# Kernel optimization log

Measured on AMD Instinct MI355X. Metric: run time of the kernel, lower is better.

The kernel has to match this reference:

```python
import jax, jax.numpy as jnp
import numpy as np

EPS = 1e-5
EXTEND_SCOPE = 1.0

def conv2d(x, w, b, pad):
    out = jax.lax.conv_general_dilated(x, w, (1, 1), [(pad, pad), (pad, pad)],
                                       dimension_numbers=('NCHW', 'OIHW', 'NCHW'))
    return out + b[None, :, None, None]

def group_norm(x, groups, gamma, beta):
    B, C, H, W = x.shape
    xg = x.reshape(B, groups, -1)
    mu = xg.mean(-1, keepdims=True)
    var = xg.var(-1, keepdims=True)
    xn = ((xg - mu) * jax.lax.rsqrt(var + EPS)).reshape(B, C, H, W)
    return xn * gamma[None, :, None, None] + beta[None, :, None, None]

def bilinear_sample(feat, y, x):
    # feat [B,C,H,W]; y,x pixel coords [B,Ho,Wo]; zeros padding, align_corners=True
    B, C, H, W = feat.shape
    flat = feat.reshape(B, C, H * W)
    y0 = jnp.floor(y); x0 = jnp.floor(x)
    wy = (y - y0)[:, None]; wx = (x - x0)[:, None]  # [B,1,Ho,Wo]
    y0i = y0.astype(jnp.int32); x0i = x0.astype(jnp.int32)
    Ho, Wo = y.shape[1], y.shape[2]
    def gather(yi, xi):
        valid = ((yi >= 0) & (yi < H) & (xi >= 0) & (xi < W)).astype(feat.dtype)[:, None]
        idx = (jnp.clip(yi, 0, H - 1) * W + jnp.clip(xi, 0, W - 1)).reshape(B, -1)
        g = jax.vmap(lambda f, i: f[:, i])(flat, idx).reshape(B, C, Ho, Wo)
        return g * valid
    g00 = gather(y0i, x0i)
    g01 = gather(y0i, x0i + 1)
    g10 = gather(y0i + 1, x0i)
    g11 = gather(y0i + 1, x0i + 1)
    return g00 * (1 - wy) * (1 - wx) + g01 * (1 - wy) * wx + g10 * wy * (1 - wx) + g11 * wy * wx

def setup_inputs() -> dict:
    key = jax.random.key(0)
    ks = jax.random.split(key, 4)
    B, C, H, W, K, O = 4, 64, 128, 128, 9, 64
    return {
        'x': jax.random.normal(ks[0], (B, C, H, W), jnp.float32),
        'w_off': jax.random.normal(ks[1], (K, C, 3, 3), jnp.float32) * 0.05,
        'b_off': jnp.zeros((K,), jnp.float32),
        'w_theta': jax.random.normal(ks[2], (K, C, 5, 5), jnp.float32) * 0.05,
        'b_theta': jnp.zeros((K,), jnp.float32),
        'gn_off_g': jnp.ones((K,), jnp.float32),
        'gn_off_b': jnp.zeros((K,), jnp.float32),
        'gn_th_g': jnp.ones((K,), jnp.float32),
        'gn_th_b': jnp.zeros((K,), jnp.float32),
        'w_strip': jax.random.normal(ks[3], (O, C, K, 1), jnp.float32) * 0.05,
        'b_strip': jnp.zeros((O,), jnp.float32),
        'gn_out_g': jnp.ones((O,), jnp.float32),
        'gn_out_b': jnp.zeros((O,), jnp.float32),
    }

def reference(x, w_off, b_off, w_theta, b_theta, gn_off_g, gn_off_b,
              gn_th_g, gn_th_b, w_strip, b_strip, gn_out_g, gn_out_b):
    B, C, H, W = x.shape
    K = w_off.shape[0]
    center = K // 2
    off = jnp.tanh(group_norm(conv2d(x, w_off, b_off, 1), 3, gn_off_g, gn_off_b))       # [B,K,H,W]
    th = jnp.arctan(group_norm(conv2d(x, w_theta, b_theta, 2), 3, gn_th_g, gn_th_b))    # [B,K,H,W]
    k = jnp.arange(K)
    s = (k - center).astype(x.dtype)[None, :, None, None]   # signed kernel offset
    m = center + jnp.abs(k - center)                        # mirror index (uses theta/offset at center+|i|)
    th_m = th[:, m]; off_m = off[:, m]                      # [B,K,H,W]
    is_center = (k == center)[None, :, None, None]
    y_off = jnp.where(is_center, 0.0, s * jnp.tan(th_m) + off_m * jnp.cos(th_m))
    x_off = jnp.where(is_center, 0.0, s - jnp.sin(th_m) * off_m)
    y_new = jnp.arange(H, dtype=x.dtype)[None, None, :, None] + s + EXTEND_SCOPE * y_off
    x_new = jnp.arange(W, dtype=x.dtype)[None, None, None, :] + s + EXTEND_SCOPE * x_off
    # rearrange 'b k h w -> b (h k) w'
    y_map = y_new.transpose(0, 2, 1, 3).reshape(B, H * K, W)
    x_map = x_new.transpose(0, 2, 1, 3).reshape(B, H * K, W)
    # clamp to valid range; scale to [-1,1] + align_corners=True grid_sample is identity in pixel space
    y_map = jnp.clip(y_map, 0.0, float(H - 1))
    x_map = jnp.clip(x_map, 0.0, float(W - 1))
    deformed = bilinear_sample(x, y_map, x_map)             # [B,C,K*H,W]
    d = deformed.reshape(B, C, H, K, W)
    out = jnp.einsum('bchkw,ock->bohw', d, w_strip[..., 0]) + b_strip[None, :, None, None]
    O = w_strip.shape[0]
    out = jax.nn.relu(group_norm(out, O // 4, gn_out_g, gn_out_b))
    return out
```

## Files before the change

kernel.cpp:

```cpp
#include <hip/hip_runtime.h>
#include <math.h>


typedef short v8s __attribute__((ext_vector_type(8)));
typedef float v4f __attribute__((ext_vector_type(4)));

__device__ __forceinline__ float fast_tanh(float a) {
    float aa = fabsf(a);
    float e = __expf(2.f * aa);
    float t = 1.f - 2.f / (e + 1.f);
    return copysignf(t, a);
}

__global__ __launch_bounds__(256) void k_pack(
    const float* __restrict__ w_strip, short* __restrict__ w_pack)
{
    int idx = blockIdx.x * 256 + threadIdx.x;
    int j    = idx & 7;
    int lane = (idx >> 3) & 63;
    int kk   = (idx >> 9) & 1;
    int wv   = (idx >> 10) & 3;
    int k    = idx >> 12;
    int c = (kk << 5) + ((lane >> 4) << 3) + j;
    int o = (wv << 4) + (lane & 15);
    union { short s; __bf16 h; } u;
    u.h = (__bf16)w_strip[(o * 64 + c) * 9 + k];
    w_pack[idx] = u.s;
}

__global__ __launch_bounds__(256) void k_tr(
    const float* __restrict__ x, float* __restrict__ xt)
{
    __shared__ float l[64][65];
    const int t    = threadIdx.x;
    const int lane = t & 63;
    const int wv   = t >> 6;
    const int b    = blockIdx.x >> 8;
    const int pix0 = (blockIdx.x & 255) << 6;

#pragma unroll
    for (int it = 0; it < 16; ++it) {
        int c = (wv << 4) + it;
        l[lane][c] = x[(((size_t)(b << 6) + c) << 14) + pix0 + lane];
    }
    __syncthreads();
#pragma unroll
    for (int it = 0; it < 4; ++it) {
        int idx = (it << 8) + t;
        int p  = idx >> 4;
        int c4 = (idx & 15) << 2;
        float4 v = { l[p][c4], l[p][c4 + 1], l[p][c4 + 2], l[p][c4 + 3] };
        *(float4*)(xt + (((size_t)(b << 14) + pix0 + p) << 6) + c4) = v;
    }
}

__global__ __launch_bounds__(256, 8) void k_conv(
    const float* __restrict__ x,
    const float* __restrict__ w_off, const float* __restrict__ b_off,
    const float* __restrict__ w_th,  const float* __restrict__ b_th,
    float* __restrict__ off_raw, float* __restrict__ th_raw)
{
    __shared__ float tile[12][36];
    const int t  = threadIdx.x;
    const int tx = t & 31, ty = t >> 5;
    const int z  = blockIdx.z;
    const int b  = z >> 3, sp = z & 7;
    const int c0 = sp << 3;
    const int h0 = blockIdx.y << 3, w0 = blockIdx.x << 5;

    float accO[9], accT[9];
#pragma unroll
    for (int k = 0; k < 9; ++k) { accO[k] = 0.f; accT[k] = 0.f; }

    for (int ci = 0; ci < 8; ++ci) {
        const int c = c0 + ci;
        __syncthreads();
        const float* xp = x + (((size_t)(b << 6) + c) << 14);
        for (int e = t; e < 432; e += 256) {
            int r = e / 36, cc = e - r * 36;
            int hh = h0 + r - 2, ww = w0 + cc - 2;
            tile[r][cc] = (hh >= 0 && hh < 128 && ww >= 0 && ww < 128)
                            ? xp[(hh << 7) + ww] : 0.f;
        }
        __syncthreads();

        float win[5][5];
#pragma unroll
        for (int i = 0; i < 5; ++i)
#pragma unroll
            for (int j = 0; j < 5; ++j)
                win[i][j] = tile[ty + i][tx + j];

#pragma unroll
        for (int k = 0; k < 9; ++k) {
            const float* wo = w_off + (size_t)((k << 6) + c) * 9;
            float a = accO[k];
#pragma unroll
            for (int i = 0; i < 3; ++i)
#pragma unroll
                for (int j = 0; j < 3; ++j)
                    a = fmaf(win[i + 1][j + 1], wo[i * 3 + j], a);
            accO[k] = a;

            const float* wt = w_th + (size_t)((k << 6) + c) * 25;
            float bb = accT[k];
#pragma unroll
            for (int i = 0; i < 5; ++i)
#pragma unroll
                for (int j = 0; j < 5; ++j)
                    bb = fmaf(win[i][j], wt[i * 5 + j], bb);
            accT[k] = bb;
        }
    }

    const int pix = ((h0 + ty) << 7) + (w0 + tx);
#pragma unroll
    for (int k = 0; k < 9; ++k) {
        float vo = accO[k] + (sp == 0 ? b_off[k] : 0.f);
        float vt = accT[k] + (sp == 0 ? b_th[k]  : 0.f);
        atomicAdd(&off_raw[((b * 9 + k) << 14) + pix], vo);
        atomicAdd(&th_raw [((b * 9 + k) << 14) + pix], vt);
    }
}

__global__ __launch_bounds__(256) void k_stats(
    const float* __restrict__ off_raw, const float* __restrict__ th_raw,
    float* __restrict__ stats)
{
    const int id  = blockIdx.x;
    const int arr = id >= 36;
    const int rem = id - arr * 36;
    const float4* src = (const float4*)((arr ? th_raw : off_raw) + (rem << 14));

    float s1 = 0.f, s2 = 0.f;
    for (int i = threadIdx.x; i < 4096; i += 256) {
        float4 v = src[i];
        s1 += v.x + v.y + v.z + v.w;
        s2 += v.x * v.x + v.y * v.y + v.z * v.z + v.w * v.w;
    }
#pragma unroll
    for (int d = 32; d; d >>= 1) { s1 += __shfl_down(s1, d, 64); s2 += __shfl_down(s2, d, 64); }

    __shared__ float ls1[4], ls2[4];
    const int wv = threadIdx.x >> 6;
    if ((threadIdx.x & 63) == 0) { ls1[wv] = s1; ls2[wv] = s2; }
    __syncthreads();
    if (threadIdx.x == 0) {
        stats[arr * 72 + rem]      = ls1[0] + ls1[1] + ls1[2] + ls1[3];
        stats[arr * 72 + 36 + rem] = ls2[0] + ls2[1] + ls2[2] + ls2[3];
    }
}

__global__ __launch_bounds__(256, 8) void k_sample_strip2(
    const float* __restrict__ xt,
    const float* __restrict__ off_raw, const float* __restrict__ th_raw,
    const float* __restrict__ stats,
    const float* __restrict__ g_off, const float* __restrict__ be_off,
    const float* __restrict__ g_th,  const float* __restrict__ be_th,
    const short* __restrict__ w_pack, const float* __restrict__ b_strip,
    float* __restrict__ out, float* __restrict__ out_stats)
{
    __shared__ __align__(16) short smem[2][2048];
    const int t    = threadIdx.x;
    const int lane = t & 63;
    const int wv   = __builtin_amdgcn_readfirstlane(t >> 6);
    const int bid  = blockIdx.x;
    const int blk  = ((bid & 7) << 8) + (bid >> 3);
    const int b    = blk >> 9;
    const int pix0 = (blk & 511) << 5;
    const int l32  = lane & 31;
    const int q    = lane >> 5;
    const int p_img = pix0 + l32;
    const int h    = p_img >> 7, w = p_img & 127;
    const int i15  = lane & 15, lg = lane >> 4;
    const int c0   = (wv << 4) + (q << 3);
    const int cb   = (wv << 1) + q;

    float muO[3], isO[3], muT[3], isT[3];
    const float inv_cnt = 1.f / (3.f * 16384.f);
#pragma unroll
    for (int g = 0; g < 3; ++g) {
        float s = 0.f, qq = 0.f;
#pragma unroll
        for (int j = 0; j < 3; ++j) { s += stats[b * 9 + 3 * g + j]; qq += stats[36 + b * 9 + 3 * g + j]; }
        float mu = s * inv_cnt;
        muO[g] = mu; isO[g] = rsqrtf(fmaxf(qq * inv_cnt - mu * mu, 0.f) + 1e-5f);
        s = 0.f; qq = 0.f;
#pragma unroll
        for (int j = 0; j < 3; ++j) { s += stats[72 + b * 9 + 3 * g + j]; qq += stats[108 + b * 9 + 3 * g + j]; }
        mu = s * inv_cnt;
        muT[g] = mu; isT[g] = rsqrtf(fmaxf(qq * inv_cnt - mu * mu, 0.f) + 1e-5f);
    }

    const float* xtb = xt + ((size_t)(b << 14) << 6);

    v4f acc[2];
    acc[0] = (v4f)0.f; acc[1] = (v4f)0.f;
    int cur = 0;

    for (int k = 0; k < 9; ++k) {
        float vv[8];
        if (k == 4) {
            const float* src = xtb + ((size_t)p_img << 6) + c0;
            float4 A = *(const float4*)src;
            float4 Bv = *(const float4*)(src + 4);
            vv[0] = A.x;  vv[1] = A.y;  vv[2] = A.z;  vv[3] = A.w;
            vv[4] = Bv.x; vv[5] = Bv.y; vv[6] = Bv.z; vv[7] = Bv.w;
        } else {
            const int s = k - 4;
            const int m = 4 + (s < 0 ? -s : s);
            const int g = m / 3;
            float z = (th_raw[((b * 9 + m) << 14) + p_img] - muT[g]) * isT[g] * g_th[m] + be_th[m];
            float f = fast_tanh((off_raw[((b * 9 + m) << 14) + p_img] - muO[g]) * isO[g] * g_off[m] + be_off[m]);
            float r = rsqrtf(1.f + z * z);
            float fs = (float)s;
            float yy = (float)h + fs + fs * z + f * r;
            float xx = (float)w + fs + fs - z * r * f;
            yy = fminf(fmaxf(yy, 0.f), 127.f);
            xx = fminf(fmaxf(xx, 0.f), 127.f);
            int y0 = min((int)yy, 126);
            int x0 = min((int)xx, 126);
            float wy = yy - (float)y0;
            float wx = xx - (float)x0;
            const float* base = xtb + ((size_t)((y0 << 7) + x0) << 6) + c0;
#pragma unroll
            for (int hf = 0; hf < 2; ++hf) {
                const float* bp = base + (hf << 2);
                float4 c00 = *(const float4*)bp;
                float4 c01 = *(const float4*)(bp + 64);
                float4 c10 = *(const float4*)(bp + 8192);
                float4 c11 = *(const float4*)(bp + 8256);
                float tx0 = fmaf(wx, c01.x - c00.x, c00.x);
                float ty0 = fmaf(wx, c01.y - c00.y, c00.y);
                float tz0 = fmaf(wx, c01.z - c00.z, c00.z);
                float tw0 = fmaf(wx, c01.w - c00.w, c00.w);
                float bx0 = fmaf(wx, c11.x - c10.x, c10.x);
                float by0 = fmaf(wx, c11.y - c10.y, c10.y);
                float bz0 = fmaf(wx, c11.z - c10.z, c10.z);
                float bw0 = fmaf(wx, c11.w - c10.w, c10.w);
                vv[hf * 4 + 0] = fmaf(wy, bx0 - tx0, tx0);
                vv[hf * 4 + 1] = fmaf(wy, by0 - ty0, ty0);
                vv[hf * 4 + 2] = fmaf(wy, bz0 - tz0, tz0);
                vv[hf * 4 + 3] = fmaf(wy, bw0 - tw0, tw0);
            }
        }

        union { v8s s8; __bf16 hh[8]; } u;
#pragma unroll
        for (int j = 0; j < 8; ++j) u.hh[j] = (__bf16)vv[j];
        *(v8s*)&smem[cur][((cb << 5) + l32) << 3] = u.s8;
        __syncthreads();

        const short* wpk = w_pack + (((k << 2) + wv) << 10) + (lane << 3);
        v8s a0 = *(const v8s*)wpk;
        v8s a1 = *(const v8s*)(wpk + 512);

#pragma unroll
        for (int n = 0; n < 2; ++n) {
            int p16 = (n << 4) + i15;
            v8s b0 = *(const v8s*)&smem[cur][((lg << 5) + p16) << 3];
            v8s b1 = *(const v8s*)&smem[cur][(((lg + 4) << 5) + p16) << 3];
            acc[n] = __builtin_amdgcn_mfma_f32_16x16x32_bf16(a0, b0, acc[n], 0, 0, 0);
            acc[n] = __builtin_amdgcn_mfma_f32_16x16x32_bf16(a1, b1, acc[n], 0, 0, 0);
        }
        cur ^= 1;
    }

#pragma unroll
    for (int r = 0; r < 4; ++r) {
        int o = (wv << 4) + (lg << 2) + r;
        float bias = b_strip[o];
        float v0 = acc[0][r] + bias;
        float v1 = acc[1][r] + bias;
        float* op = out + (((size_t)(b << 6) + o) << 14) + pix0 + i15;
        op[0]  = v0;
        op[16] = v1;
        float s1 = v0 + v1;
        float s2 = v0 * v0 + v1 * v1;
#pragma unroll
        for (int d = 1; d <= 8; d <<= 1) {
            s1 += __shfl_xor(s1, d, 64);
            s2 += __shfl_xor(s2, d, 64);
        }
        if (i15 == 0) {
            atomicAdd(&out_stats[(b << 6) + o], s1);
            atomicAdd(&out_stats[256 + (b << 6) + o], s2);
        }
    }
}

__global__ __launch_bounds__(256) void k_sample_strip_old(
    const float* __restrict__ x,
    const float* __restrict__ off_raw, const float* __restrict__ th_raw,
    const float* __restrict__ stats,
    const float* __restrict__ g_off, const float* __restrict__ be_off,
    const float* __restrict__ g_th,  const float* __restrict__ be_th,
    const short* __restrict__ w_pack, const float* __restrict__ b_strip,
    float* __restrict__ out)
{
    __shared__ __align__(16) short smem[64 * 64];
    const int t    = threadIdx.x;
    const int lane = t & 63;
    const int wv   = __builtin_amdgcn_readfirstlane(t >> 6);
    const int bid  = blockIdx.x;
    const int blk  = ((bid & 7) << 7) + (bid >> 3);
    const int b    = blk >> 8;
    const int pix0 = (blk & 255) << 6;
    const int p    = pix0 + lane;
    const int h    = p >> 7, w = p & 127;
    const int i15  = lane & 15, lg = lane >> 4;

    float muO[3], isO[3], muT[3], isT[3];
    const float inv_cnt = 1.f / (3.f * 16384.f);
#pragma unroll
    for (int g = 0; g < 3; ++g) {
        float s = 0.f, q = 0.f;
#pragma unroll
        for (int j = 0; j < 3; ++j) { s += stats[b * 9 + 3 * g + j]; q += stats[36 + b * 9 + 3 * g + j]; }
        float mu = s * inv_cnt;
        muO[g] = mu; isO[g] = rsqrtf(fmaxf(q * inv_cnt - mu * mu, 0.f) + 1e-5f);
        s = 0.f; q = 0.f;
#pragma unroll
        for (int j = 0; j < 3; ++j) { s += stats[72 + b * 9 + 3 * g + j]; q += stats[108 + b * 9 + 3 * g + j]; }
        mu = s * inv_cnt;
        muT[g] = mu; isT[g] = rsqrtf(fmaxf(q * inv_cnt - mu * mu, 0.f) + 1e-5f);
    }

    const float* xb = x + ((size_t)((b << 6) + (wv << 4)) << 14);
    v4f acc[4];
#pragma unroll
    for (int n = 0; n < 4; ++n) acc[n] = (v4f)0.f;

    for (int k = 0; k < 9; ++k) {
        float v[16];
        if (k == 4) {
#pragma unroll
            for (int ci = 0; ci < 16; ++ci) v[ci] = xb[(ci << 14) + p];
        } else {
            const int s = k - 4;
            const int m = 4 + (s < 0 ? -s : s);
            const int g = m / 3;
            float z = (th_raw[((b * 9 + m) << 14) + p] - muT[g]) * isT[g] * g_th[m] + be_th[m];
            float f = fast_tanh((off_raw[((b * 9 + m) << 14) + p] - muO[g]) * isO[g] * g_off[m] + be_off[m]);
            float r = rsqrtf(1.f + z * z);
            float fs = (float)s;
            float yy = (float)h + fs + fs * z + f * r;
            float xx = (float)w + fs + fs - z * r * f;
            yy = fminf(fmaxf(yy, 0.f), 127.f);
            xx = fminf(fmaxf(xx, 0.f), 127.f);
            int y0 = min((int)yy, 126);
            int x0 = min((int)xx, 126);
            float wy = yy - (float)y0;
            float wx = xx - (float)x0;
            const float* base = xb + (y0 << 7) + x0;
#pragma unroll
            for (int ci = 0; ci < 16; ++ci) {
                const float* qp = base + (ci << 14);
                float2 r0 = *(const float2*)qp;
                float2 r1 = *(const float2*)(qp + 128);
                float lo = fmaf(wx, r0.y - r0.x, r0.x);
                float hi = fmaf(wx, r1.y - r1.x, r1.x);
                v[ci] = fmaf(wy, hi - lo, lo);
            }
        }

        union { v8s s8; __bf16 hh[8]; } u0, u1;
#pragma unroll
        for (int ci = 0; ci < 8; ++ci) { u0.hh[ci] = (__bf16)v[ci]; u1.hh[ci] = (__bf16)v[ci + 8]; }
        *(v8s*)&smem[(lane << 6) + ((((wv << 1) + 0) + lane) & 7) * 8] = u0.s8;
        *(v8s*)&smem[(lane << 6) + ((((wv << 1) + 1) + lane) & 7) * 8] = u1.s8;
        __syncthreads();

        const short* wpk = w_pack + (((k << 2) + wv) << 10) + (lane << 3);
        v8s a0 = *(const v8s*)wpk;
        v8s a1 = *(const v8s*)(wpk + 512);

#pragma unroll
        for (int n = 0; n < 4; ++n) {
            int r = (n << 4) + i15;
            v8s b0 = *(const v8s*)&smem[(r << 6) + (((lg    ) + r) & 7) * 8];
            v8s b1 = *(const v8s*)&smem[(r << 6) + (((lg + 4) + r) & 7) * 8];
            acc[n] = __builtin_amdgcn_mfma_f32_16x16x32_bf16(a0, b0, acc[n], 0, 0, 0);
            acc[n] = __builtin_amdgcn_mfma_f32_16x16x32_bf16(a1, b1, acc[n], 0, 0, 0);
        }
        __syncthreads();
    }

#pragma unroll
    for (int r = 0; r < 4; ++r) {
        int o = (wv << 4) + (lg << 2) + r;
        float bias = b_strip[o];
        float* op = out + ((size_t)((b << 6) + o) << 14) + pix0 + i15;
#pragma unroll
        for (int n = 0; n < 4; ++n)
            op[n << 4] = acc[n][r] + bias;
    }
}

__global__ __launch_bounds__(256) void k_stats_out(
    const float* __restrict__ out, float* __restrict__ out_stats)
{
    const int bo = blockIdx.x;
    const float4* src = (const float4*)(out + ((size_t)bo << 14));
    float s1 = 0.f, s2 = 0.f;
    for (int i = threadIdx.x; i < 4096; i += 256) {
        float4 v = src[i];
        s1 += v.x + v.y + v.z + v.w;
        s2 += v.x * v.x + v.y * v.y + v.z * v.z + v.w * v.w;
    }
#pragma unroll
    for (int d = 32; d; d >>= 1) { s1 += __shfl_down(s1, d, 64); s2 += __shfl_down(s2, d, 64); }

    __shared__ float ls1[4], ls2[4];
    const int wv = threadIdx.x >> 6;
    if ((threadIdx.x & 63) == 0) { ls1[wv] = s1; ls2[wv] = s2; }
    __syncthreads();
    if (threadIdx.x == 0) {
        out_stats[bo]       = ls1[0] + ls1[1] + ls1[2] + ls1[3];
        out_stats[256 + bo] = ls2[0] + ls2[1] + ls2[2] + ls2[3];
    }
}

__global__ __launch_bounds__(256) void k_gn_out(
    float* __restrict__ out, const float* __restrict__ out_stats,
    const float* __restrict__ gg, const float* __restrict__ gb)
{
    const float inv_cnt = 1.f / (4.f * 16384.f);
    const int n4 = 1 << 20;
    for (int idx = blockIdx.x * 256 + threadIdx.x; idx < n4; idx += gridDim.x * 256) {
        int flat = idx << 2;
        int ch = (flat >> 14) & 63;
        int b  = flat >> 20;
        int cb = (b << 6) + ((ch >> 2) << 2);
        float s = out_stats[cb] + out_stats[cb + 1] + out_stats[cb + 2] + out_stats[cb + 3];
        float q = out_stats[256 + cb] + out_stats[256 + cb + 1] + out_stats[256 + cb + 2] + out_stats[256 + cb + 3];
        float mu   = s * inv_cnt;
        float istd = rsqrtf(fmaxf(q * inv_cnt - mu * mu, 0.f) + 1e-5f);
        float ga = gg[ch] * istd;
        float be = gb[ch] - mu * ga;
        float4 v = *reinterpret_cast<float4*>(out + flat);
        v.x = fmaxf(fmaf(v.x, ga, be), 0.f);
        v.y = fmaxf(fmaf(v.y, ga, be), 0.f);
        v.z = fmaxf(fmaf(v.z, ga, be), 0.f);
        v.w = fmaxf(fmaf(v.w, ga, be), 0.f);
        *reinterpret_cast<float4*>(out + flat) = v;
    }
}

extern "C" void kernel_launch(void* const* d_in, const int* in_sizes, int n_in,
                              void* d_out, int out_size, void* d_ws, size_t ws_size,
                              hipStream_t stream)
{
    const float* x       = (const float*)d_in[0];
    const float* w_off   = (const float*)d_in[1];
    const float* b_off   = (const float*)d_in[2];
    const float* w_th    = (const float*)d_in[3];
    const float* b_th    = (const float*)d_in[4];
    const float* g_off   = (const float*)d_in[5];
    const float* be_off  = (const float*)d_in[6];
    const float* g_th    = (const float*)d_in[7];
    const float* be_th   = (const float*)d_in[8];
    const float* w_strip = (const float*)d_in[9];
    const float* b_strip = (const float*)d_in[10];
    const float* gg      = (const float*)d_in[11];
    const float* gb      = (const float*)d_in[12];

    float* out       = (float*)d_out;
    float* ws        = (float*)d_ws;
    float* off_raw   = ws;
    float* th_raw    = ws + 589824;
    float* stats     = ws + 1179648;
    float* out_stats = ws + 1179792;
    short* w_pack    = (short*)(ws + 1180304);
    float* xt        = ws + 1198736;

    const size_t need_full = (size_t)(1198736 + 4194304) * sizeof(float);
    const bool big = ws_size >= need_full;

    hipMemsetAsync(ws, 0, (size_t)1180304 * sizeof(float), stream);

    k_pack<<<144, 256, 0, stream>>>(w_strip, w_pack);
    if (big) k_tr<<<1024, 256, 0, stream>>>(x, xt);
    dim3 g1(4, 16, 32);
    k_conv<<<g1, 256, 0, stream>>>(x, w_off, b_off, w_th, b_th, off_raw, th_raw);
    k_stats<<<72, 256, 0, stream>>>(off_raw, th_raw, stats);
    if (big) {
        k_sample_strip2<<<2048, 256, 0, stream>>>(xt, off_raw, th_raw, stats,
                                                  g_off, be_off, g_th, be_th,
                                                  w_pack, b_strip, out, out_stats);
    } else {
        k_sample_strip_old<<<1024, 256, 0, stream>>>(x, off_raw, th_raw, stats,
                                                     g_off, be_off, g_th, be_th,
                                                     w_pack, b_strip, out);
        k_stats_out<<<256, 256, 0, stream>>>(out, out_stats);
    }
    k_gn_out<<<4096, 256, 0, stream>>>(out, out_stats, gg, gb);
}
```

Before: 192.3 us.

## Restructure sample-strip kernel so each wave owns pixels and feeds MFMA directly

The sampling+strip-conv kernel is reorganized so each wave handles 16 pixels across all 64 channels and all 64 outputs. Bilinear samples are converted to bf16 and passed straight into the MFMA B operand, which removes the shared-memory staging and per-tap __syncthreads. Gather loads and weight fragments for the next half-tap are prefetched in registers while the current one is computed, and the deformation parameters are precomputed once for the four mirrored taps. The cost is higher register use (launch bounds lowered to 4 blocks) and more atomics per block for the output statistics.

```diff
diff --git a/kernel.cpp b/kernel.cpp
--- a/kernel.cpp
+++ b/kernel.cpp
@@ -19,10 +19,10 @@
     int j    = idx & 7;
     int lane = (idx >> 3) & 63;
     int kk   = (idx >> 9) & 1;
-    int wv   = (idx >> 10) & 3;
+    int og   = (idx >> 10) & 3;
     int k    = idx >> 12;
     int c = (kk << 5) + ((lane >> 4) << 3) + j;
-    int o = (wv << 4) + (lane & 15);
+    int o = (og << 4) + (lane & 15);
     union { short s; __bf16 h; } u;
     u.h = (__bf16)w_strip[(o * 64 + c) * 9 + k];
     w_pack[idx] = u.s;
@@ -151,7 +151,7 @@
     }
 }
 
-__global__ __launch_bounds__(256, 8) void k_sample_strip2(
+__global__ __launch_bounds__(256, 4) void k_sample_mfma(
     const float* __restrict__ xt,
     const float* __restrict__ off_raw, const float* __restrict__ th_raw,
     const float* __restrict__ stats,
@@ -160,131 +160,158 @@
     const short* __restrict__ w_pack, const float* __restrict__ b_strip,
     float* __restrict__ out, float* __restrict__ out_stats)
 {
-    __shared__ __align__(16) short smem[2][2048];
     const int t    = threadIdx.x;
     const int lane = t & 63;
-    const int wv   = __builtin_amdgcn_readfirstlane(t >> 6);
+    const int wv   = t >> 6;
+    const int i15  = lane & 15, lg = lane >> 4;
     const int bid  = blockIdx.x;
-    const int blk  = ((bid & 7) << 8) + (bid >> 3);
-    const int b    = blk >> 9;
-    const int pix0 = (blk & 511) << 5;
-    const int l32  = lane & 31;
-    const int q    = lane >> 5;
-    const int p_img = pix0 + l32;
-    const int h    = p_img >> 7, w = p_img & 127;
-    const int i15  = lane & 15, lg = lane >> 4;
-    const int c0   = (wv << 4) + (q << 3);
-    const int cb   = (wv << 1) + q;
-
-    float muO[3], isO[3], muT[3], isT[3];
+    const int blk  = ((bid & 7) << 7) + (bid >> 3);
+    const int b    = blk >> 8;
+    const int pix0 = (blk & 255) << 6;
+    const int pp   = pix0 + (wv << 4) + i15;
+    const int h    = pp >> 7, w = pp & 127;
+    const int cg   = lg << 3;
+
     const float inv_cnt = 1.f / (3.f * 16384.f);
-#pragma unroll
-    for (int g = 0; g < 3; ++g) {
-        float s = 0.f, qq = 0.f;
-#pragma unroll
-        for (int j = 0; j < 3; ++j) { s += stats[b * 9 + 3 * g + j]; qq += stats[36 + b * 9 + 3 * g + j]; }
-        float mu = s * inv_cnt;
-        muO[g] = mu; isO[g] = rsqrtf(fmaxf(qq * inv_cnt - mu * mu, 0.f) + 1e-5f);
-        s = 0.f; qq = 0.f;
-#pragma unroll
-        for (int j = 0; j < 3; ++j) { s += stats[72 + b * 9 + 3 * g + j]; qq += stats[108 + b * 9 + 3 * g + j]; }
-        mu = s * inv_cnt;
-        muT[g] = mu; isT[g] = rsqrtf(fmaxf(qq * inv_cnt - mu * mu, 0.f) + 1e-5f);
-    }
-
-    const float* xtb = xt + ((size_t)(b << 14) << 6);
-
-    v4f acc[2];
-    acc[0] = (v4f)0.f; acc[1] = (v4f)0.f;
-    int cur = 0;
-
-    for (int k = 0; k < 9; ++k) {
-        float vv[8];
-        if (k == 4) {
-            const float* src = xtb + ((size_t)p_img << 6) + c0;
-            float4 A = *(const float4*)src;
-            float4 Bv = *(const float4*)(src + 4);
-            vv[0] = A.x;  vv[1] = A.y;  vv[2] = A.z;  vv[3] = A.w;
-            vv[4] = Bv.x; vv[5] = Bv.y; vv[6] = Bv.z; vv[7] = Bv.w;
-        } else {
-            const int s = k - 4;
-            const int m = 4 + (s < 0 ? -s : s);
-            const int g = m / 3;
-            float z = (th_raw[((b * 9 + m) << 14) + p_img] - muT[g]) * isT[g] * g_th[m] + be_th[m];
-            float f = fast_tanh((off_raw[((b * 9 + m) << 14) + p_img] - muO[g]) * isO[g] * g_off[m] + be_off[m]);
-            float r = rsqrtf(1.f + z * z);
-            float fs = (float)s;
-            float yy = (float)h + fs + fs * z + f * r;
-            float xx = (float)w + fs + fs - z * r * f;
-            yy = fminf(fmaxf(yy, 0.f), 127.f);
-            xx = fminf(fmaxf(xx, 0.f), 127.f);
-            int y0 = min((int)yy, 126);
-            int x0 = min((int)xx, 126);
-            float wy = yy - (float)y0;
-            float wx = xx - (float)x0;
-            const float* base = xtb + ((size_t)((y0 << 7) + x0) << 6) + c0;
-#pragma unroll
-            for (int hf = 0; hf < 2; ++hf) {
-                const float* bp = base + (hf << 2);
-                float4 c00 = *(const float4*)bp;
-                float4 c01 = *(const float4*)(bp + 64);
-                float4 c10 = *(const float4*)(bp + 8192);
-                float4 c11 = *(const float4*)(bp + 8256);
-                float tx0 = fmaf(wx, c01.x - c00.x, c00.x);
-                float ty0 = fmaf(wx, c01.y - c00.y, c00.y);
-                float tz0 = fmaf(wx, c01.z - c00.z, c00.z);
-                float tw0 = fmaf(wx, c01.w - c00.w, c00.w);
-                float bx0 = fmaf(wx, c11.x - c10.x, c10.x);
-                float by0 = fmaf(wx, c11.y - c10.y, c10.y);
-                float bz0 = fmaf(wx, c11.z - c10.z, c10.z);
-                float bw0 = fmaf(wx, c11.w - c10.w, c10.w);
-                vv[hf * 4 + 0] = fmaf(wy, bx0 - tx0, tx0);
-                vv[hf * 4 + 1] = fmaf(wy, by0 - ty0, ty0);
-                vv[hf * 4 + 2] = fmaf(wy, bz0 - tz0, tz0);
-                vv[hf * 4 + 3] = fmaf(wy, bw0 - tw0, tw0);
+    float muO1, isO1, muT1, isT1, muO2, isO2, muT2, isT2;
+    {
+        float s, q, mu;
+        s = stats[b*9+3] + stats[b*9+4] + stats[b*9+5];
+        q = stats[36+b*9+3] + stats[36+b*9+4] + stats[36+b*9+5];
+        mu = s * inv_cnt; muO1 = mu;
+        isO1 = rsqrtf(fmaxf(q * inv_cnt - mu * mu, 0.f) + 1e-5f);
+        s = stats[b*9+6] + stats[b*9+7] + stats[b*9+8];
+        q = stats[36+b*9+6] + stats[36+b*9+7] + stats[36+b*9+8];
+        mu = s * inv_cnt; muO2 = mu;
+        isO2 = rsqrtf(fmaxf(q * inv_cnt - mu * mu, 0.f) + 1e-5f);
+        s = stats[72+b*9+3] + stats[72+b*9+4] + stats[72+b*9+5];
+        q = stats[108+b*9+3] + stats[108+b*9+4] + stats[108+b*9+5];
+        mu = s * inv_cnt; muT1 = mu;
+        isT1 = rsqrtf(fmaxf(q * inv_cnt - mu * mu, 0.f) + 1e-5f);
+        s = stats[72+b*9+6] + stats[72+b*9+7] + stats[72+b*9+8];
+        q = stats[108+b*9+6] + stats[108+b*9+7] + stats[108+b*9+8];
+        mu = s * inv_cnt; muT2 = mu;
+        isT2 = rsqrtf(fmaxf(q * inv_cnt - mu * mu, 0.f) + 1e-5f);
+    }
+
+    float zt[4], cyv[4], cxv[4];
+#pragma unroll
+    for (int m = 5; m <= 8; ++m) {
+        const int mi = m - 5;
+        float tv = th_raw [((b * 9 + m) << 14) + pp];
+        float ov = off_raw[((b * 9 + m) << 14) + pp];
+        float muT = (m == 5) ? muT1 : muT2, isT = (m == 5) ? isT1 : isT2;
+        float muO = (m == 5) ? muO1 : muO2, isO = (m == 5) ? isO1 : isO2;
+        float z = (tv - muT) * isT * g_th[m] + be_th[m];
+        float f = fast_tanh((ov - muO) * isO * g_off[m] + be_off[m]);
+        float r = rsqrtf(1.f + z * z);
+        zt[mi]  = z;
+        cyv[mi] = f * r;
+        cxv[mi] = z * r * f;
+    }
+
+    const float* xtb = xt + ((size_t)b << 20);
+
+    float4 L[8];
+    v8s Af[2][4];
+    float cwy = 0.f, cwx = 0.f;
+    int  cidx = 0;
+
+    {
+        float yy = (float)h - 4.f - 4.f * zt[3] + cyv[3];
+        float xx = (float)w - 8.f - cxv[3];
+        yy = fminf(fmaxf(yy, 0.f), 127.f);
+        xx = fminf(fmaxf(xx, 0.f), 127.f);
+        int y0 = min((int)yy, 126), x0 = min((int)xx, 126);
+        cwy = yy - (float)y0; cwx = xx - (float)x0;
+        cidx = (y0 << 7) + x0;
+        const float* bb = xtb + ((size_t)cidx << 6) + cg;
+        L[0] = *(const float4*)bb;        L[1] = *(const float4*)(bb + 4);
+        L[2] = *(const float4*)(bb + 64); L[3] = *(const float4*)(bb + 68);
+        L[4] = *(const float4*)(bb + 8192); L[5] = *(const float4*)(bb + 8196);
+        L[6] = *(const float4*)(bb + 8256); L[7] = *(const float4*)(bb + 8260);
+        const short* wa = w_pack + (lane << 3);
+#pragma unroll
+        for (int og = 0; og < 4; ++og)
+            Af[0][og] = *(const v8s*)(wa + (og << 10));
+    }
+
+    v4f acc[4];
+#pragma unroll
+    for (int og = 0; og < 4; ++og) acc[og] = (v4f)0.f;
+
+#pragma unroll
+    for (int r = 0; r < 18; ++r) {
+        float vj[8];
+#pragma unroll
+        for (int j = 0; j < 8; ++j) {
+            float c00 = (j < 4) ? L[0][j] : L[1][j - 4];
+            float c01 = (j < 4) ? L[2][j] : L[3][j - 4];
+            float c10 = (j < 4) ? L[4][j] : L[5][j - 4];
+            float c11 = (j < 4) ? L[6][j] : L[7][j - 4];
+            float top = fmaf(cwx, c01 - c00, c00);
+            float bot = fmaf(cwx, c11 - c10, c10);
+            vj[j] = fmaf(cwy, bot - top, top);
+        }
+
+        if (r < 17) {
+            const int rn = r + 1;
+            const int k2 = rn >> 1, kk2 = rn & 1;
+            if (kk2 == 0) {
+                float yy, xx;
+                if (k2 == 4) {
+                    yy = (float)h; xx = (float)w;
+                } else {
+                    const int s  = k2 - 4;
+                    const int mi = (s < 0 ? -s : s) - 1;
+                    const float fs = (float)s;
+                    yy = (float)h + fs + fs * zt[mi] + cyv[mi];
+                    xx = (float)w + 2.f * fs - cxv[mi];
+                    yy = fminf(fmaxf(yy, 0.f), 127.f);
+                    xx = fminf(fmaxf(xx, 0.f), 127.f);
+                }
+                int y0 = min((int)yy, 126), x0 = min((int)xx, 126);
+                cwy = yy - (float)y0; cwx = xx - (float)x0;
+                cidx = (y0 << 7) + x0;
             }
+            const float* bb = xtb + ((size_t)cidx << 6) + (kk2 << 5) + cg;
+            L[0] = *(const float4*)bb;        L[1] = *(const float4*)(bb + 4);
+            L[2] = *(const float4*)(bb + 64); L[3] = *(const float4*)(bb + 68);
+            L[4] = *(const float4*)(bb + 8192); L[5] = *(const float4*)(bb + 8196);
+            L[6] = *(const float4*)(bb + 8256); L[7] = *(const float4*)(bb + 8260);
+            const short* wa = w_pack + (((k2 << 3) + kk2) << 9) + (lane << 3);
+#pragma unroll
+            for (int og = 0; og < 4; ++og)
+                Af[rn & 1][og] = *(const v8s*)(wa + (og << 10));
         }
 
         union { v8s s8; __bf16 hh[8]; } u;
 #pragma unroll
-        for (int j = 0; j < 8; ++j) u.hh[j] = (__bf16)vv[j];
-        *(v8s*)&smem[cur][((cb << 5) + l32) << 3] = u.s8;
-        __syncthreads();
-
-        const short* wpk = w_pack + (((k << 2) + wv) << 10) + (lane << 3);
-        v8s a0 = *(const v8s*)wpk;
-        v8s a1 = *(const v8s*)(wpk + 512);
-
-#pragma unroll
-        for (int n = 0; n < 2; ++n) {
-            int p16 = (n << 4) + i15;
-            v8s b0 = *(const v8s*)&smem[cur][((lg << 5) + p16) << 3];
-            v8s b1 = *(const v8s*)&smem[cur][(((lg + 4) << 5) + p16) << 3];
-            acc[n] = __builtin_amdgcn_mfma_f32_16x16x32_bf16(a0, b0, acc[n], 0, 0, 0);
-            acc[n] = __builtin_amdgcn_mfma_f32_16x16x32_bf16(a1, b1, acc[n], 0, 0, 0);
-        }
-        cur ^= 1;
-    }
-
-#pragma unroll
-    for (int r = 0; r < 4; ++r) {
-        int o = (wv << 4) + (lg << 2) + r;
-        float bias = b_strip[o];
-        float v0 = acc[0][r] + bias;
-        float v1 = acc[1][r] + bias;
-        float* op = out + (((size_t)(b << 6) + o) << 14) + pix0 + i15;
-        op[0]  = v0;
-        op[16] = v1;
-        float s1 = v0 + v1;
-        float s2 = v0 * v0 + v1 * v1;
-#pragma unroll
-        for (int d = 1; d <= 8; d <<= 1) {
-            s1 += __shfl_xor(s1, d, 64);
-            s2 += __shfl_xor(s2, d, 64);
-        }
-        if (i15 == 0) {
-            atomicAdd(&out_stats[(b << 6) + o], s1);
-            atomicAdd(&out_stats[256 + (b << 6) + o], s2);
+        for (int j = 0; j < 8; ++j) u.hh[j] = (__bf16)vj[j];
+
+#pragma unroll
+        for (int og = 0; og < 4; ++og)
+            acc[og] = __builtin_amdgcn_mfma_f32_16x16x32_bf16(
+                          Af[r & 1][og], u.s8, acc[og], 0, 0, 0);
+    }
+
+#pragma unroll
+    for (int og = 0; og < 4; ++og) {
+#pragma unroll
+        for (int r = 0; r < 4; ++r) {
+            int o = (og << 4) + (lg << 2) + r;
+            float val = acc[og][r] + b_strip[o];
+            out[(((size_t)(b << 6) + o) << 14) + pp] = val;
+            float s1 = val, s2 = val * val;
+#pragma unroll
+            for (int d = 1; d <= 8; d <<= 1) {
+                s1 += __shfl_xor(s1, d, 64);
+                s2 += __shfl_xor(s2, d, 64);
+            }
+            if (i15 == 0) {
+                atomicAdd(&out_stats[(b << 6) + o], s1);
+                atomicAdd(&out_stats[256 + (b << 6) + o], s2);
+            }
         }
     }
 }
@@ -485,9 +512,9 @@
     k_conv<<<g1, 256, 0, stream>>>(x, w_off, b_off, w_th, b_th, off_raw, th_raw);
     k_stats<<<72, 256, 0, stream>>>(off_raw, th_raw, stats);
     if (big) {
-        k_sample_strip2<<<2048, 256, 0, stream>>>(xt, off_raw, th_raw, stats,
-                                                  g_off, be_off, g_th, be_th,
-                                                  w_pack, b_strip, out, out_stats);
+        k_sample_mfma<<<1024, 256, 0, stream>>>(xt, off_raw, th_raw, stats,
+                                                g_off, be_off, g_th, be_th,
+                                                w_pack, b_strip, out, out_stats);
     } else {
         k_sample_strip_old<<<1024, 256, 0, stream>>>(x, off_raw, th_raw, stats,
                                                      g_off, be_off, g_th, be_th,
```

New measurement: 254.7 us. 1.32x slower.
